# Optimization experiments

Measured on AMD Instinct MI355X. Metric: run time of the kernel, lower is better.

## Reference

```python
import jax, jax.numpy as jnp
import numpy as np
import math

EPS = 1e-8
H, DM, S = 16, 1024, 128  # heads, d_model, seq_len (== channels)
DK = DM // H


def _fq_act_uint8(x):
    # Brevitas Uint8ActPerTensorFloat: per-tensor unsigned 8-bit fake-quant (negatives clip to 0)
    s = jnp.maximum(jnp.max(x), EPS) / 255.0
    return jnp.clip(jnp.round(x / s), 0.0, 255.0) * s


def _fq_w_int8(w):
    # Int8 weight per-tensor, narrow range [-127, 127]
    s = jnp.maximum(jnp.max(jnp.abs(w)), EPS) / 127.0
    return jnp.clip(jnp.round(w / s), -127.0, 127.0) * s, s


def _fq_pc_int8(x, axis):
    # QuantIdentity: signed 8-bit fake-quant, per-channel scale along `axis` (abs-max stats)
    red = tuple(i for i in range(x.ndim) if i != axis)
    s = jnp.maximum(jnp.max(jnp.abs(x), axis=red, keepdims=True), EPS) / 127.0
    return jnp.clip(jnp.round(x / s), -128.0, 127.0) * s


def _quant_linear(x, W, b):
    # QuantLinear: uint8 input quant, int8 weight quant, Int32 bias quant (scale = s_in * s_w)
    s_in = jnp.maximum(jnp.max(x), EPS) / 255.0
    xq = jnp.clip(jnp.round(x / s_in), 0.0, 255.0) * s_in
    Wq, s_w = _fq_w_int8(W)
    s_b = s_in * s_w
    bq = jnp.round(b / s_b) * s_b
    return jnp.einsum('bsd,od->bso', xq, Wq) + bq


def setup_inputs() -> dict:
    key = jax.random.key(0)
    ks = jax.random.split(key, 12)
    B = 64
    std = 1.0 / math.sqrt(DM)
    inp = {
        'query': jax.random.normal(ks[0], (B, S, DM), jnp.float32),
        'key':   jax.random.normal(ks[1], (B, S, DM), jnp.float32),
        'value': jax.random.normal(ks[2], (B, S, DM), jnp.float32),
        'mask':  jnp.ones((B, S, S), jnp.int32),
    }
    for i, nm in enumerate(['q', 'k', 'v', 'o']):
        inp[f'W{nm}'] = jax.random.normal(ks[3 + i], (DM, DM), jnp.float32) * std
        inp[f'b{nm}'] = jax.random.normal(ks[7 + i], (DM,), jnp.float32) * 0.01
    return inp


def reference(query, key, value, mask, Wq, bq, Wk, bk, Wv, bv, Wo, bo):
    B = query.shape[0]
    # QuantLinear projections -> [B, h, S, d_k]
    def proj(x, W, b):
        return _quant_linear(x, W, b).reshape(B, S, H, DK).transpose(0, 2, 1, 3)
    q = proj(query, Wq, bq)
    k = proj(key, Wk, bk)
    v = proj(value, Wv, bv)

    # quantizer_1: per-channel on q rows (axis 2); quantizer_2: on k^T columns (axis 3)
    kt = jnp.swapaxes(k, -2, -1)  # [B, h, d_k, S]
    scores = jnp.matmul(_fq_pc_int8(q, 2), _fq_pc_int8(kt, 3)) / math.sqrt(DK)
    scores = jnp.where(mask[:, None, :, :] == 0, -1e9, scores)
    p_attn = jax.nn.softmax(scores, axis=-1)

    # quantizer_3: per-channel on p_attn columns (axis 3); quantizer_4: on v rows (axis 2)
    x = jnp.matmul(_fq_pc_int8(p_attn, 3), _fq_pc_int8(v, 2))  # [B, h, S, d_k]
    x = x.transpose(0, 2, 1, 3).reshape(B, S, DM)
    return _quant_linear(x, Wo, bo)
```

## Files before the change

kernel.cpp:

```cpp
#include <hip/hip_runtime.h>
#include <hip/hip_bf16.h>
#include <math.h>

typedef unsigned short u16;
typedef unsigned int u32;
typedef unsigned long long u64;
typedef signed char i8;

constexpr int NB = 64, NS = 128, NDM = 1024, NH = 16, NDK = 64;
constexpr int NM = NB * NS;
constexpr float QEPS = 1e-8f;

typedef __attribute__((ext_vector_type(8))) short short8;
typedef __attribute__((ext_vector_type(4))) float f32x4;
typedef __attribute__((ext_vector_type(4))) int i32x4;

__device__ __forceinline__ u32 fenc(float f) {
  u32 u = __float_as_uint(f);
  return (u & 0x80000000u) ? ~u : (u | 0x80000000u);
}
__device__ __forceinline__ float fdec(u32 u) {
  u = (u & 0x80000000u) ? (u & 0x7FFFFFFFu) : ~u;
  return __uint_as_float(u);
}
__device__ __forceinline__ u16 f2bf(float f) { return (u16)(__float_as_uint(f) >> 16); }
__device__ __forceinline__ float bf2f(u16 u) { return __uint_as_float(((u32)u) << 16); }

__device__ __forceinline__ void glds16(const void* g, void* l) {
  __builtin_amdgcn_global_load_lds(
      (const __attribute__((address_space(1))) void*)(unsigned long long)(uintptr_t)g,
      (__attribute__((address_space(3))) void*)(u32)(uintptr_t)l, 16, 0, 0);
}


__global__ void maskbits_kernel(const int* __restrict__ mask, u64* __restrict__ mb,
                                u32* __restrict__ scl) {
  if (blockIdx.x == 0) {
    for (int i = threadIdx.x; i < 2048; i += blockDim.x) scl[i] = 0u;
  }
  int row = blockIdx.x * 4 + (threadIdx.x >> 6);
  int lane = threadIdx.x & 63;
  const int* mrow = mask + (size_t)row * NS;
  u64 b0 = __ballot(mrow[lane] != 0);
  u64 b1 = __ballot(mrow[64 + lane] != 0);
  if (lane == 0) { mb[row * 2] = b0; mb[row * 2 + 1] = b1; }
}

__global__ void fused_max_kernel(const float* __restrict__ q, const float* __restrict__ k,
                                 const float* __restrict__ v, const float* __restrict__ w0,
                                 const float* __restrict__ w1, const float* __restrict__ w2,
                                 const float* __restrict__ w3, u32* __restrict__ sclu) {
  int y = blockIdx.y;
  const float* src; size_t n4; int ab;
  switch (y) {
    case 0: src = q; n4 = (size_t)NM * NDM / 4; ab = 0; break;
    case 1: src = k; n4 = (size_t)NM * NDM / 4; ab = 0; break;
    case 2: src = v; n4 = (size_t)NM * NDM / 4; ab = 0; break;
    case 3: src = w0; n4 = (size_t)NDM * NDM / 4; ab = 1; break;
    case 4: src = w1; n4 = (size_t)NDM * NDM / 4; ab = 1; break;
    case 5: src = w2; n4 = (size_t)NDM * NDM / 4; ab = 1; break;
    default: src = w3; n4 = (size_t)NDM * NDM / 4; ab = 1; break;
  }
  float m = -INFINITY;
  size_t stride = (size_t)gridDim.x * blockDim.x;
  for (size_t i = (size_t)blockIdx.x * blockDim.x + threadIdx.x; i < n4; i += stride) {
    float4 f = ((const float4*)src)[i];
    if (ab) { f.x = fabsf(f.x); f.y = fabsf(f.y); f.z = fabsf(f.z); f.w = fabsf(f.w); }
    m = fmaxf(m, fmaxf(fmaxf(f.x, f.y), fmaxf(f.z, f.w)));
  }
  for (int off = 32; off; off >>= 1) m = fmaxf(m, __shfl_down(m, off));
  __shared__ float sm[4];
  if ((threadIdx.x & 63) == 0) sm[threadIdx.x >> 6] = m;
  __syncthreads();
  if (threadIdx.x == 0) {
    float r = fmaxf(fmaxf(sm[0], sm[1]), fmaxf(sm[2], sm[3]));
    atomicMax(&sclu[y], fenc(r));
  }
}

__global__ __launch_bounds__(256)
void quant_w_i8_kernel(const float* __restrict__ w0, const float* __restrict__ w1,
                       const float* __restrict__ w2, const float* __restrict__ w3,
                       i8* __restrict__ dst, int* __restrict__ colsum,
                       const u32* __restrict__ sclu) {
  int y = blockIdx.y, row = blockIdx.x, tid = threadIdx.x;
  const float* src = (y == 0 ? w0 : y == 1 ? w1 : y == 2 ? w2 : w3) + (size_t)row * NDM;
  float s = fmaxf(fdec(sclu[3 + y]), QEPS) / 127.0f;
  float4 f = ((const float4*)src)[tid];
  int a = (int)fminf(fmaxf(rintf(f.x / s), -127.f), 127.f);
  int b = (int)fminf(fmaxf(rintf(f.y / s), -127.f), 127.f);
  int c = (int)fminf(fmaxf(rintf(f.z / s), -127.f), 127.f);
  int d = (int)fminf(fmaxf(rintf(f.w / s), -127.f), 127.f);
  ((int*)(dst + (size_t)y * NDM * NDM + (size_t)row * NDM))[tid] =
      (a & 255) | ((b & 255) << 8) | ((c & 255) << 16) | ((d & 255) << 24);
  int ssum = a + b + c + d;
  for (int off = 32; off; off >>= 1) ssum += __shfl_down(ssum, off);
  __shared__ int sm[4];
  if ((tid & 63) == 0) sm[tid >> 6] = ssum;
  __syncthreads();
  if (tid == 0) colsum[y * NDM + row] = sm[0] + sm[1] + sm[2] + sm[3];
}

__global__ void quant_a_kernel(const float* __restrict__ s0, const float* __restrict__ s1,
                               const float* __restrict__ s2, i8* __restrict__ dst,
                               const u32* __restrict__ sclu, int slot_base) {
  int y = blockIdx.y;
  const float* src = y == 0 ? s0 : y == 1 ? s1 : s2;
  i8* d = dst + (size_t)y * NM * NDM;
  float s = fmaxf(fdec(sclu[slot_base + y]), QEPS) / 255.0f;
  size_t n4 = (size_t)NM * NDM / 4;
  size_t stride = (size_t)gridDim.x * blockDim.x;
  for (size_t i = (size_t)blockIdx.x * blockDim.x + threadIdx.x; i < n4; i += stride) {
    float4 f = ((const float4*)src)[i];
    int a = (int)fminf(fmaxf(rintf(f.x / s), 0.f), 255.f) - 128;
    int b = (int)fminf(fmaxf(rintf(f.y / s), 0.f), 255.f) - 128;
    int c = (int)fminf(fmaxf(rintf(f.z / s), 0.f), 255.f) - 128;
    int e = (int)fminf(fmaxf(rintf(f.w / s), 0.f), 255.f) - 128;
    ((int*)d)[i] = (a & 255) | ((b & 255) << 8) | ((c & 255) << 16) | ((e & 255) << 24);
  }
}

__global__ void qkv_i8_kernel(const float* __restrict__ projbase, i8* __restrict__ dstbase,
                              const float* __restrict__ scl) {
  int y = blockIdx.y;
  const float* src = projbase + (size_t)y * NM * NDM;
  i8* dst = dstbase + (size_t)y * NM * NDM;
  const float* sb = scl + 8 + y * 128;
  size_t n4 = (size_t)NM * NDM / 4;
  size_t stride = (size_t)gridDim.x * blockDim.x;
  for (size_t i = (size_t)blockIdx.x * blockDim.x + threadIdx.x; i < n4; i += stride) {
    int s_idx = (int)((i >> 8) & 127);
    float s = fmaxf(sb[s_idx], QEPS) / 127.0f;
    float4 f = ((const float4*)src)[i];
    int a = (int)fminf(fmaxf(rintf(f.x / s), -128.f), 127.f);
    int b = (int)fminf(fmaxf(rintf(f.y / s), -128.f), 127.f);
    int c = (int)fminf(fmaxf(rintf(f.z / s), -128.f), 127.f);
    int d = (int)fminf(fmaxf(rintf(f.w / s), -128.f), 127.f);
    ((int*)dst)[i] = (a & 255) | ((b & 255) << 8) | ((c & 255) << 16) | ((d & 255) << 24);
  }
}

constexpr int BM = 128, BN = 128, BK = 64;

template <bool PROJ>
__global__ __launch_bounds__(256)
void gemm_kernel(const i8* __restrict__ Abase, const i8* __restrict__ Wbase,
                 const int* __restrict__ colsum, const float* __restrict__ b0,
                 const float* __restrict__ b1, const float* __restrict__ b2,
                 float* __restrict__ Cbase, u32* __restrict__ sclu) {
  constexpr int K = NDM, N = NDM;
  const int z = PROJ ? blockIdx.z : 0;
  const i8* A = Abase + (size_t)z * NM * NDM;
  const i8* Wt = PROJ ? (Wbase + (size_t)z * NDM * NDM) : Wbase;
  const float* bias = PROJ ? (z == 0 ? b0 : z == 1 ? b1 : b2) : b0;
  float* C = PROJ ? (Cbase + (size_t)z * NM * NDM) : Cbase;
  const u32* slot_in = PROJ ? (sclu + z) : (sclu + 7);
  const u32* slot_w = PROJ ? (sclu + 3 + z) : (sclu + 6);
  const int* cs = colsum + (PROJ ? z : 3) * NDM;

  __shared__ __align__(16) i8 As[BM][BK];
  __shared__ __align__(16) i8 Bs[BN][BK];
  __shared__ float rmax2[2][BM];

  const int tid = threadIdx.x;
  const int lane = tid & 63, wave = tid >> 6;
  const int wm = (wave & 1) * 64, wn = (wave >> 1) * 64;
  const int r16 = lane & 15, quad = lane >> 4;
  const int bm = blockIdx.x * BM, bn = blockIdx.y * BN;

  i32x4 acc[4][4] = {};

  const int lrow = lane >> 2, lcol = (lane & 3) * 16;
  for (int k0 = 0; k0 < K; k0 += BK) {
    __syncthreads();
#pragma unroll
    for (int p = 0; p < 2; p++) {
      int r = wave * 32 + p * 16;
      glds16(A + (size_t)(bm + r + lrow) * K + k0 + lcol, &As[r][0]);
      glds16(Wt + (size_t)(bn + r + lrow) * K + k0 + lcol, &Bs[r][0]);
    }
    __syncthreads();
    i32x4 af[4], bfr[4];
#pragma unroll
    for (int i = 0; i < 4; i++) af[i] = *(const i32x4*)(&As[wm + i * 16 + r16][quad * 16]);
#pragma unroll
    for (int j = 0; j < 4; j++) bfr[j] = *(const i32x4*)(&Bs[wn + j * 16 + r16][quad * 16]);
#pragma unroll
    for (int i = 0; i < 4; i++)
#pragma unroll
      for (int j = 0; j < 4; j++)
        acc[i][j] = __builtin_amdgcn_mfma_i32_16x16x64_i8(af[i], bfr[j], acc[i][j], 0, 0, 0);
  }

  float s_in = fmaxf(fdec(*slot_in), QEPS) / 255.0f;
  float s_w = fmaxf(fdec(*slot_w), QEPS) / 127.0f;
  float sc = s_in * s_w;

  float bq[4];
  int csj[4];
#pragma unroll
  for (int j = 0; j < 4; j++) {
    int gc = bn + wn + j * 16 + r16;
    bq[j] = rintf(bias[gc] / sc) * sc;
    csj[j] = cs[gc] << 7;
  }
#pragma unroll
  for (int i = 0; i < 4; i++) {
#pragma unroll
    for (int r = 0; r < 4; r++) {
      int lr = wm + i * 16 + quad * 4 + r;
      int gr = bm + lr;
      float rm = 0.0f;
#pragma unroll
      for (int j = 0; j < 4; j++) {
        int gc = bn + wn + j * 16 + r16;
        float val = (float)(acc[i][j][r] + csj[j]) * sc + bq[j];
        C[(size_t)gr * N + gc] = val;
        if (PROJ) rm = fmaxf(rm, fabsf(val));
      }
      if (PROJ) {
#pragma unroll
        for (int off = 1; off < 16; off <<= 1) rm = fmaxf(rm, __shfl_xor(rm, off));
        if (r16 == 0) rmax2[wave >> 1][lr] = rm;
      }
    }
  }
  if (PROJ) {
    __syncthreads();
    if (tid < BM) {
      float m = fmaxf(rmax2[0][tid], rmax2[1][tid]);
      atomicMax((int*)&sclu[8 + z * 128 + tid], __float_as_int(m));
    }
  }
}

__global__ __launch_bounds__(256)
void attn_colmax_kernel(const i8* __restrict__ qi8, const i8* __restrict__ ki8,
                        const u64* __restrict__ mb, const float* __restrict__ scl,
                        u32* __restrict__ sclu) {
  const int bh = blockIdx.x, b = bh >> 4, h = bh & 15;
  const int tid = threadIdx.x, lane = tid & 63, wave = tid >> 6;
  const int r16 = lane & 15, quad = lane >> 4;

  __shared__ __align__(16) i8 Qs[NS][80];
  __shared__ __align__(16) i8 Ks[NS][80];
  __shared__ float sqv[NS], skv[NS];
  __shared__ float cmw[4][NS];

  {
    int row = tid >> 1, half = (tid & 1) * 32;
    const i8* qp = qi8 + (size_t)(b * NS + row) * NDM + h * NDK + half;
    const i8* kp = ki8 + (size_t)(b * NS + row) * NDM + h * NDK + half;
    *(int4*)&Qs[row][half] = *(const int4*)qp;
    *(int4*)&Qs[row][half + 16] = *(const int4*)(qp + 16);
    *(int4*)&Ks[row][half] = *(const int4*)kp;
    *(int4*)&Ks[row][half + 16] = *(const int4*)(kp + 16);
    if (tid < NS) {
      sqv[tid] = fmaxf(scl[8 + tid], QEPS) / 127.0f;
      skv[tid] = fmaxf(scl[8 + 128 + tid], QEPS) / 127.0f;
    }
  }
  __syncthreads();

  const int rowbase = wave * 32;
  i32x4 acc[2][8] = {};
#pragma unroll
  for (int mt = 0; mt < 2; mt++) {
    i32x4 a = *(const i32x4*)&Qs[rowbase + mt * 16 + r16][quad * 16];
#pragma unroll
    for (int nt = 0; nt < 8; nt++) {
      i32x4 bfrag = *(const i32x4*)&Ks[nt * 16 + r16][quad * 16];
      acc[mt][nt] = __builtin_amdgcn_mfma_i32_16x16x64_i8(a, bfrag, acc[mt][nt], 0, 0, 0);
    }
  }

  float skc[8], cm[8];
#pragma unroll
  for (int nt = 0; nt < 8; nt++) { skc[nt] = skv[nt * 16 + r16]; cm[nt] = 0.0f; }

#pragma unroll
  for (int mt = 0; mt < 2; mt++) {
#pragma unroll
    for (int r = 0; r < 4; r++) {
      int row = rowbase + mt * 16 + quad * 4 + r;
      float sq = sqv[row];
      const u64* mrow = mb + ((size_t)b * NS + row) * 2;
      u64 m0 = mrow[0], m1 = mrow[1];
      float vals[8];
      float mx = -INFINITY;
#pragma unroll
      for (int nt = 0; nt < 8; nt++) {
        float v = (float)acc[mt][nt][r] * (sq * skc[nt]) * 0.125f;
        u64 bits = nt < 4 ? m0 : m1;
        if (((bits >> ((nt * 16 + r16) & 63)) & 1ull) == 0) v = -1e9f;
        vals[nt] = v;
        mx = fmaxf(mx, v);
      }
#pragma unroll
      for (int off = 1; off < 16; off <<= 1) mx = fmaxf(mx, __shfl_xor(mx, off));
      float sum = 0.0f;
#pragma unroll
      for (int nt = 0; nt < 8; nt++) { vals[nt] = __expf(vals[nt] - mx); sum += vals[nt]; }
#pragma unroll
      for (int off = 1; off < 16; off <<= 1) sum += __shfl_xor(sum, off);
#pragma unroll
      for (int nt = 0; nt < 8; nt++) {
        float p = vals[nt] / sum;
        cm[nt] = fmaxf(cm[nt], p);
      }
    }
  }

#pragma unroll
  for (int nt = 0; nt < 8; nt++) {
    float c = cm[nt];
    c = fmaxf(c, __shfl_xor(c, 16));
    c = fmaxf(c, __shfl_xor(c, 32));
    if (quad == 0) cmw[wave][nt * 16 + r16] = c;
  }
  __syncthreads();
  if (tid < NS) {
    float c = fmaxf(fmaxf(cmw[0][tid], cmw[1][tid]), fmaxf(cmw[2][tid], cmw[3][tid]));
    atomicMax((int*)&sclu[392 + tid], __float_as_int(c));
  }
}

__global__ __launch_bounds__(256, 4)
void attn_pv2_kernel(const i8* __restrict__ qi8, const i8* __restrict__ ki8,
                     const i8* __restrict__ vi8, const u64* __restrict__ mb,
                     const float* __restrict__ scl, float* __restrict__ xout,
                     u32* __restrict__ xmax_slot) {
  const int bh = blockIdx.x, b = bh >> 4, h = bh & 15;
  const int tid = threadIdx.x, lane = tid & 63, wave = tid >> 6;
  const int r16 = lane & 15, quad = lane >> 4;
  const int rowbase = wave * 32;

  union SU {
    i8 K[NS][80];
    struct { u16 hi[64][72]; u16 lo[64][72]; } v;
  };
  __shared__ __align__(16) SU u;
  __shared__ __align__(16) u16 Ps[NS][72];
  __shared__ float sqv[NS], skv[NS], spv[NS], svv[NS];

  i32x4 aq[2];
  {
    int row = tid >> 1, half = (tid & 1) * 32;
    const i8* kp = ki8 + (size_t)(b * NS + row) * NDM + h * NDK + half;
    *(int4*)&u.K[row][half] = *(const int4*)kp;
    *(int4*)&u.K[row][half + 16] = *(const int4*)(kp + 16);
    const i8* qp = qi8 + (size_t)b * NS * NDM + h * NDK;
#pragma unroll
    for (int mt = 0; mt < 2; mt++)
      aq[mt] = *(const i32x4*)(qp + (size_t)(rowbase + mt * 16 + r16) * NDM + quad * 16);
    if (tid < NS) {
      sqv[tid] = fmaxf(scl[8 + tid], QEPS) / 127.0f;
      skv[tid] = fmaxf(scl[8 + 128 + tid], QEPS) / 127.0f;
      spv[tid] = fmaxf(scl[392 + tid], QEPS) / 127.0f;
      svv[tid] = fmaxf(scl[8 + 256 + tid], QEPS) / 127.0f;
    }
  }
  __syncthreads();

  i32x4 acc[2][8] = {};
#pragma unroll
  for (int mt = 0; mt < 2; mt++) {
#pragma unroll
    for (int nt = 0; nt < 8; nt++) {
      i32x4 bfrag = *(const i32x4*)&u.K[nt * 16 + r16][quad * 16];
      acc[mt][nt] = __builtin_amdgcn_mfma_i32_16x16x64_i8(aq[mt], bfrag, acc[mt][nt], 0, 0, 0);
    }
  }

  float skc[8], spc[8];
#pragma unroll
  for (int nt = 0; nt < 8; nt++) {
    skc[nt] = skv[nt * 16 + r16];
    spc[nt] = spv[nt * 16 + r16];
  }

  u32 pqh[2][4][2];
#pragma unroll
  for (int mt = 0; mt < 2; mt++) {
#pragma unroll
    for (int r = 0; r < 4; r++) {
      int row = rowbase + mt * 16 + quad * 4 + r;
      float sq = sqv[row];
      const u64* mrow = mb + ((size_t)b * NS + row) * 2;
      u64 m0 = mrow[0], m1 = mrow[1];
      float vals[8];
      float mx = -INFINITY;
#pragma unroll
      for (int nt = 0; nt < 8; nt++) {
        float v = (float)acc[mt][nt][r] * (sq * skc[nt]) * 0.125f;
        u64 bits = nt < 4 ? m0 : m1;
        if (((bits >> ((nt * 16 + r16) & 63)) & 1ull) == 0) v = -1e9f;
        vals[nt] = v;
        mx = fmaxf(mx, v);
      }
#pragma unroll
      for (int off = 1; off < 16; off <<= 1) mx = fmaxf(mx, __shfl_xor(mx, off));
      float sum = 0.0f;
#pragma unroll
      for (int nt = 0; nt < 8; nt++) { vals[nt] = __expf(vals[nt] - mx); sum += vals[nt]; }
#pragma unroll
      for (int off = 1; off < 16; off <<= 1) sum += __shfl_xor(sum, off);
#pragma unroll
      for (int nt = 0; nt < 4; nt++) {
        float p = vals[nt] / sum;
        float pq = fminf(fmaxf(rintf(p / spc[nt]), -128.f), 127.f);
        Ps[row][nt * 16 + r16] = f2bf(pq);
      }
#pragma unroll
      for (int n2 = 0; n2 < 2; n2++) {
        float pa_ = vals[4 + n2 * 2] / sum;
        float pb_ = vals[5 + n2 * 2] / sum;
        float qa = fminf(fmaxf(rintf(pa_ / spc[4 + n2 * 2]), -128.f), 127.f);
        float qb = fminf(fmaxf(rintf(pb_ / spc[5 + n2 * 2]), -128.f), 127.f);
        pqh[mt][r][n2] = (u32)f2bf(qa) | ((u32)f2bf(qb) << 16);
      }
    }
  }

  f32x4 xacc[2][4] = {};
#pragma unroll
  for (int half = 0; half < 2; half++) {
    __syncthreads();
    {
      int jl = tid >> 2, d0 = (tid & 3) * 16;
      int j = half * 64 + jl;
      float g = spv[j] * svv[j];
      const i8* vp = vi8 + (size_t)(b * NS + j) * NDM + h * NDK + d0;
      int4 raw = *(const int4*)vp;
      const i8* rb = (const i8*)&raw;
#pragma unroll
      for (int d = 0; d < 16; d++) {
        float w = (float)rb[d] * g;
        u16 hi = f2bf(w);
        u.v.hi[d0 + d][jl] = hi;
        u.v.lo[d0 + d][jl] = f2bf(w - bf2f(hi));
      }
    }
    __syncthreads();
#pragma unroll
    for (int kk = 0; kk < 2; kk++) {
      short8 pa[2];
#pragma unroll
      for (int mt = 0; mt < 2; mt++)
        pa[mt] = *(const short8*)&Ps[rowbase + mt * 16 + r16][kk * 32 + quad * 8];
#pragma unroll
      for (int nt = 0; nt < 4; nt++) {
        short8 vh = *(const short8*)&u.v.hi[nt * 16 + r16][kk * 32 + quad * 8];
        short8 vl = *(const short8*)&u.v.lo[nt * 16 + r16][kk * 32 + quad * 8];
#pragma unroll
        for (int mt = 0; mt < 2; mt++) {
          xacc[mt][nt] = __builtin_amdgcn_mfma_f32_16x16x32_bf16(pa[mt], vh, xacc[mt][nt], 0, 0, 0);
          xacc[mt][nt] = __builtin_amdgcn_mfma_f32_16x16x32_bf16(pa[mt], vl, xacc[mt][nt], 0, 0, 0);
        }
      }
    }
    if (half == 0) {
#pragma unroll
      for (int mt = 0; mt < 2; mt++)
#pragma unroll
        for (int r = 0; r < 4; r++) {
          int row = rowbase + mt * 16 + quad * 4 + r;
#pragma unroll
          for (int n2 = 0; n2 < 2; n2++) {
            u32 pk = pqh[mt][r][n2];
            Ps[row][(n2 * 2) * 16 + r16] = (u16)(pk & 0xFFFFu);
            Ps[row][(n2 * 2 + 1) * 16 + r16] = (u16)(pk >> 16);
          }
        }
    }
  }

  float mx = -INFINITY;
#pragma unroll
  for (int mt = 0; mt < 2; mt++)
#pragma unroll
    for (int nt = 0; nt < 4; nt++)
#pragma unroll
      for (int r = 0; r < 4; r++) {
        int row = rowbase + mt * 16 + quad * 4 + r;
        xout[((size_t)b * NS + row) * NDM + h * NDK + nt * 16 + r16] = xacc[mt][nt][r];
        mx = fmaxf(mx, xacc[mt][nt][r]);
      }
#pragma unroll
  for (int off = 1; off < 64; off <<= 1) mx = fmaxf(mx, __shfl_xor(mx, off));
  if (lane == 0) atomicMax(xmax_slot, fenc(mx));
}

constexpr size_t OFF_SCL = 0;
constexpr size_t OFF_CS  = 8192;
constexpr size_t OFF_MB  = OFF_CS + 4 * NDM * 4;
constexpr size_t OFF_W   = OFF_MB + (size_t)NM * 16;
constexpr size_t OFF_XQ  = OFF_W + 4 * (size_t)NDM * NDM;
constexpr size_t OFF_PQ  = OFF_XQ + 3 * (size_t)NM * NDM;
constexpr size_t OFF_I8  = OFF_PQ + 3 * (size_t)NM * NDM * 4;

extern "C" void kernel_launch(void* const* d_in, const int* in_sizes, int n_in,
                              void* d_out, int out_size, void* d_ws, size_t ws_size,
                              hipStream_t stream) {
  const float* query = (const float*)d_in[0];
  const float* key = (const float*)d_in[1];
  const float* value = (const float*)d_in[2];
  const int* mask = (const int*)d_in[3];
  const float* Wq = (const float*)d_in[4]; const float* bq = (const float*)d_in[5];
  const float* Wk = (const float*)d_in[6]; const float* bk = (const float*)d_in[7];
  const float* Wv = (const float*)d_in[8]; const float* bv = (const float*)d_in[9];
  const float* Wo = (const float*)d_in[10]; const float* bo = (const float*)d_in[11];

  char* ws = (char*)d_ws;
  float* scl = (float*)(ws + OFF_SCL);
  u32* sclu = (u32*)scl;
  int* colsum = (int*)(ws + OFF_CS);
  u64* mb = (u64*)(ws + OFF_MB);
  i8* wb = (i8*)(ws + OFF_W);
  i8* wob = wb + 3 * (size_t)NDM * NDM;
  i8* xq = (i8*)(ws + OFF_XQ);
  float* proj = (float*)(ws + OFF_PQ);
  i8* qkv8 = (i8*)(ws + OFF_I8);
  float* xout = proj + 2 * (size_t)NM * NDM;
  i8* vi8 = qkv8 + 2 * (size_t)NM * NDM;

  maskbits_kernel<<<NM / 4, 256, 0, stream>>>(mask, mb, sclu);
  fused_max_kernel<<<dim3(512, 7), 256, 0, stream>>>(query, key, value, Wq, Wk, Wv, Wo, sclu);
  quant_w_i8_kernel<<<dim3(NDM, 4), 256, 0, stream>>>(Wq, Wk, Wv, Wo, wb, colsum, sclu);
  quant_a_kernel<<<dim3(512, 3), 256, 0, stream>>>(query, key, value, xq, sclu, 0);

  gemm_kernel<true><<<dim3(NM / BM, NDM / BN, 3), 256, 0, stream>>>(
      xq, wb, colsum, bq, bk, bv, proj, sclu);

  qkv_i8_kernel<<<dim3(512, 3), 256, 0, stream>>>(proj, qkv8, scl);

  attn_colmax_kernel<<<NB * NH, 256, 0, stream>>>(qkv8, qkv8 + (size_t)NM * NDM, mb, scl,
                                                  sclu);
  attn_pv2_kernel<<<NB * NH, 256, 0, stream>>>(qkv8, qkv8 + (size_t)NM * NDM, vi8, mb, scl,
                                               xout, sclu + 7);

  quant_a_kernel<<<dim3(512, 1), 256, 0, stream>>>(xout, xout, xout, xq, sclu, 7);
  gemm_kernel<false><<<dim3(NM / BM, NDM / BN, 1), 256, 0, stream>>>(
      xq, wob, colsum, bo, bo, bo, (float*)d_out, sclu);
}
```

Baseline: 423.4 us.

## Replace colmax atomics with partial reduction and prefetch V/K in attention

```diff
diff --git a/kernel.cpp b/kernel.cpp
--- a/kernel.cpp
+++ b/kernel.cpp
@@ -237,7 +237,7 @@
 __global__ __launch_bounds__(256)
 void attn_colmax_kernel(const i8* __restrict__ qi8, const i8* __restrict__ ki8,
                         const u64* __restrict__ mb, const float* __restrict__ scl,
-                        u32* __restrict__ sclu) {
+                        float* __restrict__ cm_part) {
   const int bh = blockIdx.x, b = bh >> 4, h = bh & 15;
   const int tid = threadIdx.x, lane = tid & 63, wave = tid >> 6;
   const int r16 = lane & 15, quad = lane >> 4;
@@ -321,8 +321,22 @@
   __syncthreads();
   if (tid < NS) {
     float c = fmaxf(fmaxf(cmw[0][tid], cmw[1][tid]), fmaxf(cmw[2][tid], cmw[3][tid]));
-    atomicMax((int*)&sclu[392 + tid], __float_as_int(c));
-  }
+    cm_part[(size_t)tid * (NB * NH) + bh] = c;
+  }
+}
+
+__global__ void colmax_reduce_kernel(const float* __restrict__ cm_part,
+                                     u32* __restrict__ sclu) {
+  int j = blockIdx.x;
+  const float* row = cm_part + (size_t)j * (NB * NH);
+  float m = 0.0f;
+  for (int i = threadIdx.x; i < NB * NH; i += blockDim.x) m = fmaxf(m, row[i]);
+  for (int off = 32; off; off >>= 1) m = fmaxf(m, __shfl_down(m, off));
+  __shared__ float sm[4];
+  if ((threadIdx.x & 63) == 0) sm[threadIdx.x >> 6] = m;
+  __syncthreads();
+  if (threadIdx.x == 0)
+    sclu[392 + j] = __float_as_uint(fmaxf(fmaxf(sm[0], sm[1]), fmaxf(sm[2], sm[3])));
 }
 
 __global__ __launch_bounds__(256, 4)
@@ -336,23 +350,31 @@
   const int rowbase = wave * 32;
 
   union SU {
-    i8 K[NS][80];
+    i8 K[NS][64];
     struct { u16 hi[64][72]; u16 lo[64][72]; } v;
   };
   __shared__ __align__(16) SU u;
   __shared__ __align__(16) u16 Ps[NS][72];
   __shared__ float sqv[NS], skv[NS], spv[NS], svv[NS];
+  __shared__ float xmw[4];
+
+  const int jl = tid >> 2, d0v = (tid & 3) * 16;
+  const i8* vb = vi8 + (size_t)(b * NS + jl) * NDM + h * NDK + d0v;
+  int4 vpre0 = *(const int4*)vb;
+  int4 vpre1 = *(const int4*)(vb + (size_t)64 * NDM);
 
   i32x4 aq[2];
   {
-    int row = tid >> 1, half = (tid & 1) * 32;
-    const i8* kp = ki8 + (size_t)(b * NS + row) * NDM + h * NDK + half;
-    *(int4*)&u.K[row][half] = *(const int4*)kp;
-    *(int4*)&u.K[row][half + 16] = *(const int4*)(kp + 16);
     const i8* qp = qi8 + (size_t)b * NS * NDM + h * NDK;
 #pragma unroll
     for (int mt = 0; mt < 2; mt++)
       aq[mt] = *(const i32x4*)(qp + (size_t)(rowbase + mt * 16 + r16) * NDM + quad * 16);
+    const int lrow = lane >> 2, lcol = (lane & 3) * 16;
+#pragma unroll
+    for (int p = 0; p < 2; p++) {
+      int r = wave * 32 + p * 16;
+      glds16(ki8 + (size_t)(b * NS + r + lrow) * NDM + h * NDK + lcol, &u.K[r][0]);
+    }
     if (tid < NS) {
       sqv[tid] = fmaxf(scl[8 + tid], QEPS) / 127.0f;
       skv[tid] = fmaxf(scl[8 + 128 + tid], QEPS) / 127.0f;
@@ -363,6 +385,7 @@
   __syncthreads();
 
   i32x4 acc[2][8] = {};
+  __builtin_amdgcn_s_setprio(1);
 #pragma unroll
   for (int mt = 0; mt < 2; mt++) {
 #pragma unroll
@@ -371,6 +394,7 @@
       acc[mt][nt] = __builtin_amdgcn_mfma_i32_16x16x64_i8(aq[mt], bfrag, acc[mt][nt], 0, 0, 0);
     }
   }
+  __builtin_amdgcn_s_setprio(0);
 
   float skc[8], spc[8];
 #pragma unroll
@@ -427,21 +451,20 @@
   for (int half = 0; half < 2; half++) {
     __syncthreads();
     {
-      int jl = tid >> 2, d0 = (tid & 3) * 16;
       int j = half * 64 + jl;
       float g = spv[j] * svv[j];
-      const i8* vp = vi8 + (size_t)(b * NS + j) * NDM + h * NDK + d0;
-      int4 raw = *(const int4*)vp;
+      int4 raw = half ? vpre1 : vpre0;
       const i8* rb = (const i8*)&raw;
 #pragma unroll
       for (int d = 0; d < 16; d++) {
         float w = (float)rb[d] * g;
         u16 hi = f2bf(w);
-        u.v.hi[d0 + d][jl] = hi;
-        u.v.lo[d0 + d][jl] = f2bf(w - bf2f(hi));
+        u.v.hi[d0v + d][jl] = hi;
+        u.v.lo[d0v + d][jl] = f2bf(w - bf2f(hi));
       }
     }
     __syncthreads();
+    __builtin_amdgcn_s_setprio(1);
 #pragma unroll
     for (int kk = 0; kk < 2; kk++) {
       short8 pa[2];
@@ -459,6 +482,7 @@
         }
       }
     }
+    __builtin_amdgcn_s_setprio(0);
     if (half == 0) {
 #pragma unroll
       for (int mt = 0; mt < 2; mt++)
@@ -488,7 +512,12 @@
       }
 #pragma unroll
   for (int off = 1; off < 64; off <<= 1) mx = fmaxf(mx, __shfl_xor(mx, off));
-  if (lane == 0) atomicMax(xmax_slot, fenc(mx));
+  if (lane == 0) xmw[wave] = mx;
+  __syncthreads();
+  if (tid == 0) {
+    float m = fmaxf(fmaxf(xmw[0], xmw[1]), fmaxf(xmw[2], xmw[3]));
+    atomicMax(xmax_slot, fenc(m));
+  }
 }
 
 constexpr size_t OFF_SCL = 0;
@@ -498,6 +527,7 @@
 constexpr size_t OFF_XQ  = OFF_W + 4 * (size_t)NDM * NDM;
 constexpr size_t OFF_PQ  = OFF_XQ + 3 * (size_t)NM * NDM;
 constexpr size_t OFF_I8  = OFF_PQ + 3 * (size_t)NM * NDM * 4;
+constexpr size_t OFF_CM  = OFF_I8 + 3 * (size_t)NM * NDM;
 
 extern "C" void kernel_launch(void* const* d_in, const int* in_sizes, int n_in,
                               void* d_out, int out_size, void* d_ws, size_t ws_size,
@@ -521,6 +551,7 @@
   i8* xq = (i8*)(ws + OFF_XQ);
   float* proj = (float*)(ws + OFF_PQ);
   i8* qkv8 = (i8*)(ws + OFF_I8);
+  float* cm_part = (float*)(ws + OFF_CM);
   float* xout = proj + 2 * (size_t)NM * NDM;
   i8* vi8 = qkv8 + 2 * (size_t)NM * NDM;
 
@@ -535,7 +566,8 @@
   qkv_i8_kernel<<<dim3(512, 3), 256, 0, stream>>>(proj, qkv8, scl);
 
   attn_colmax_kernel<<<NB * NH, 256, 0, stream>>>(qkv8, qkv8 + (size_t)NM * NDM, mb, scl,
-                                                  sclu);
+                                                  cm_part);
+  colmax_reduce_kernel<<<NS, 256, 0, stream>>>(cm_part, sclu);
   attn_pv2_kernel<<<NB * NH, 256, 0, stream>>>(qkv8, qkv8 + (size_t)NM * NDM, vi8, mb, scl,
                                                xout, sclu + 7);
 
```

Result: faster. 388.5 us (-8.2%).
